# Optimization experiments

Hardware: AMD Instinct MI355X
Metric: run time of the kernel (lower is better)

## Reference

```python
import jax, jax.numpy as jnp
import numpy as np
from jax import lax


def _depthwise_conv1d(x, w, b):
    # x: [B, L, D]; w: [D, 1, KW]; b: [D]
    # Mirrors torch nn.Conv1d(D, D, kernel_size=4, groups=D, padding=3): output length L + 3.
    D = x.shape[-1]
    xt = jnp.transpose(x, (0, 2, 1))  # [B, D, L]
    out = lax.conv_general_dilated(
        xt, w, window_strides=(1,), padding=[(3, 3)],
        feature_group_count=D, dimension_numbers=('NCH', 'OIH', 'NCH'))
    return jnp.transpose(out + b[None, :, None], (0, 2, 1))  # [B, L+3, D]


def _forward(x, a_hat, W_U, W_B, b_B, W_C, b_C, W_d1, b_d1, W_d2, b_d2, D_skip, conv_w, conv_b):
    xc = _depthwise_conv1d(x, conv_w, conv_b)            # [B, Lc, D], Lc = L + 3
    Bsz, Lc, Dm = xc.shape
    S = a_hat.shape[0]
    # selective parameters (torch Linear: y = x @ W.T + b)
    dt_feat = jax.nn.silu(xc @ W_d1.T + b_d1)            # [B, Lc, R]
    delta = jax.nn.softplus(dt_feat @ W_d2.T + b_d2)     # [B, Lc, 1]
    logA = -jnp.exp(a_hat)                               # [S], log(A) <= 0
    A_t = jnp.exp(delta * logA)                          # [B, Lc, S] discretized transition
    u_t = xc @ W_U.T                                     # [B, Lc, S]
    B_t = (xc @ W_B.T + b_B) * u_t                       # [B, Lc, S]
    C_t = xc @ W_C.T + b_C                               # [B, Lc, S]

    # selective scan: h_t = A_t * h_{t-1} + B_t * u_t ; y_t = <C_t, h_t> + D_skip * u_t
    # state h is per-(batch, channel d): [B, D, S]
    def step(h, inp):
        A_l, B_l, C_l, u_l = inp                         # [B,S],[B,S],[B,S],[B,D]
        h = A_l[:, None, :] * h + B_l[:, None, :] * u_l[:, :, None]  # [B, D, S]
        y = jnp.einsum('bds,bs->bd', h, C_l) + D_skip[None, :] * u_l
        return h, y

    h0 = jnp.zeros((Bsz, Dm, S), dtype=xc.dtype)
    _, ys = lax.scan(step, h0, (jnp.swapaxes(A_t, 0, 1), jnp.swapaxes(B_t, 0, 1),
                                jnp.swapaxes(C_t, 0, 1), jnp.swapaxes(xc, 0, 1)))
    return jnp.swapaxes(ys, 0, 1)                        # [B, Lc, D]


def setup_inputs() -> dict:
    key = jax.random.key(0)
    ks = jax.random.split(key, 10)
    B, L, D, S, R, KW = 4, 2048, 1024, 64, 4, 4
    f = jnp.float32
    sc = 0.02
    return {
        'x': jax.random.normal(ks[0], (B, L, D), f),
        'a_hat': jax.random.normal(ks[1], (S,), f),
        'W_U': jax.random.normal(ks[2], (S, D), f) * sc,
        'W_B': jax.random.normal(ks[3], (S, D), f) * sc,
        'b_B': jnp.zeros((S,), f),
        'W_C': jax.random.normal(ks[4], (S, D), f) * sc,
        'b_C': jnp.zeros((S,), f),
        'W_d1': jax.random.normal(ks[5], (R, D), f) * sc,
        'b_d1': jnp.zeros((R,), f),
        'W_d2': jax.random.normal(ks[6], (1, R), f) * sc,
        'b_d2': jnp.zeros((1,), f),
        'D_skip': jax.random.normal(ks[7], (D,), f),
        'conv_w': jax.random.normal(ks[8], (D, 1, KW), f) * 0.25,
        'conv_b': jnp.zeros((D,), f),
    }


def reference(x, a_hat, W_U, W_B, b_B, W_C, b_C, W_d1, b_d1, W_d2, b_d2, D_skip, conv_w, conv_b):
    return _forward(x, a_hat, W_U, W_B, b_B, W_C, b_C, W_d1, b_d1, W_d2, b_d2, D_skip, conv_w, conv_b)
```

## Files before the change

kernel.cpp:

```cpp
#include <hip/hip_runtime.h>
#include <hip/hip_bf16.h>

namespace {
constexpr int kB   = 4;
constexpr int kL   = 2048;
constexpr int kLc  = 2051;
constexpr int kD   = 1024;
constexpr int kS   = 64;
constexpr int kM   = kB * kLc;
constexpr int kNR  = 256;
constexpr int kQ   = 32;
constexpr int kTC  = (kLc + kQ - 1) / kQ;
constexpr int kGA  = 514;
constexpr int kGT  = 16384;
}

typedef __attribute__((ext_vector_type(8))) short bf16x8;
typedef __attribute__((ext_vector_type(4))) float f32x4;
typedef __attribute__((ext_vector_type(8))) unsigned short u16x8;

__device__ __forceinline__ float siluf_(float v) {
  return v / (1.f + expf(-v));
}
__device__ __forceinline__ float softplusf_(float v) {
  return (v > 20.f) ? v : log1pf(expf(v));
}
__device__ __forceinline__ unsigned short f2bf_(float f) {
  unsigned u = __float_as_uint(f);
  unsigned r = u + 0x7FFF + ((u >> 16) & 1);
  return (unsigned short)(r >> 16);
}
__device__ __forceinline__ float bf2f_(unsigned short u) {
  return __uint_as_float(((unsigned)u) << 16);
}

__global__ __launch_bounds__(256) void conv_kernel(
    const float* __restrict__ x, const float* __restrict__ cw,
    const float* __restrict__ cb, unsigned short* __restrict__ xcp,
    unsigned short* __restrict__ xT,
    const float* __restrict__ W_U, const float* __restrict__ W_B,
    const float* __restrict__ W_C, const float* __restrict__ W_d1,
    unsigned short* __restrict__ wcp) {
  __shared__ unsigned short tileT[kQ][136];

  int tid = threadIdx.x;
  if (blockIdx.y == 8) {
    int bx = blockIdx.x;
    if (bx < 128) {
      int g = bx >> 3, kq = bx & 7;
      int c8 = tid & 15, r = tid >> 4;
      int n = g * 16 + r;
      int k = kq * 128 + c8 * 8;
      const float* src = nullptr;
      if (n < 64)        src = W_U + (size_t)n * kD;
      else if (n < 128)  src = W_B + (size_t)(n - 64) * kD;
      else if (n < 192)  src = W_C + (size_t)(n - 128) * kD;
      else if (n < 196)  src = W_d1 + (size_t)(n - 192) * kD;
      u16x8 o;
#pragma unroll
      for (int j = 0; j < 8; ++j)
        o[j] = src ? f2bf_(src[k + j]) : (unsigned short)0;
      size_t dst = (size_t)g * kGT + (size_t)(k >> 5) * 512 + r * 32 + (k & 31);
      *(u16x8*)(wcp + dst) = o;
    } else if (bx < 136) {
      u16x8 z = {0, 0, 0, 0, 0, 0, 0, 0};
      size_t off = (size_t)513 * kGT + (size_t)(bx - 128) * 2048 + (size_t)tid * 8;
      *(u16x8*)(xcp + off) = z;
    } else if (bx < 138) {
      int i = (bx - 136) * 256 + tid;
      int kt = i >> 4, rr = (i >> 2) & 3, k8 = i & 3;
      u16x8 z = {0, 0, 0, 0, 0, 0, 0, 0};
      size_t off = (size_t)512 * kGT + (size_t)kt * 512 + (12 + rr) * 32 + k8 * 8;
      *(u16x8*)(xcp + off) = z;
    }
    return;
  }

  int bc = blockIdx.x;
  int d0 = blockIdx.y * 128;
  int b = bc / kTC, c = bc % kTC;
  int t0 = c * kQ;
  int dl = tid & 127, tg = tid >> 7;
  int d = d0 + dl;

  float4 wv = *(const float4*)(cw + (size_t)d * 4);
  float bias = cb[d];
  int tstart = t0 + tg * 16;

  const float* xb = x + (size_t)b * kL * kD + d;
  auto ldx = [&](int t) -> float {
    return (t >= 0 && t < kL) ? xb[(size_t)t * kD] : 0.f;
  };
  float xm3 = ldx(tstart - 3);
  float xm2 = ldx(tstart - 2);
  float xm1 = ldx(tstart - 1);

  unsigned short vals[16];
#pragma unroll
  for (int j = 0; j < 16; ++j) {
    int t = tstart + j;
    float x0 = ldx(t);
    float o = bias + wv.x * xm3 + wv.y * xm2 + wv.z * xm1 + wv.w * x0;
    vals[j] = (t < kLc) ? f2bf_(o) : (unsigned short)0;
    tileT[tg * 16 + j][dl] = vals[j];
    xm3 = xm2; xm2 = xm1; xm1 = x0;
  }
#pragma unroll
  for (int j = 0; j < 16; ++j) {
    int t = tstart + j;
    if (t < kLc) {
      int bt = b * kLc + t;
      size_t po = (size_t)(bt >> 4) * kGT + (size_t)(d >> 5) * 512 +
                  (size_t)(bt & 15) * 32 + (d & 31);
      xcp[po] = vals[j];
    }
  }
  __syncthreads();
  {
    int d_l = tid >> 1, th = tid & 1;
    u16x8 o0, o1;
#pragma unroll
    for (int j = 0; j < 8; ++j) {
      o0[j] = tileT[th * 16 + j][d_l];
      o1[j] = tileT[th * 16 + 8 + j][d_l];
    }
    unsigned short* dst = xT + ((size_t)bc * kD + d0 + d_l) * kQ + th * 16;
    *(u16x8*)dst = o0;
    *(u16x8*)(dst + 8) = o1;
  }
}

__global__ __launch_bounds__(256) void gemm_mfma_kernel(
    const unsigned short* __restrict__ xcp,
    const unsigned short* __restrict__ wcp, float* __restrict__ raw) {
  int tid = threadIdx.x;
  int w = tid >> 6, lane = tid & 63;
  int m0 = blockIdx.x * 32 + (w >> 1) * 16;
  int n0 = (w & 1) * 128;
  int l15 = lane & 15, lk = lane >> 4;

  const unsigned short* ap =
      xcp + (size_t)(blockIdx.x * 2 + (w >> 1)) * kGT + l15 * 32 + lk * 8;
  const unsigned short* bp =
      wcp + (size_t)((w & 1) * 8) * kGT + l15 * 32 + lk * 8;

  f32x4 acc[8];
#pragma unroll
  for (int nf = 0; nf < 8; ++nf) acc[nf] = f32x4{0.f, 0.f, 0.f, 0.f};

  bf16x8 a = *(const bf16x8*)(ap);
  bf16x8 bfr[8];
#pragma unroll
  for (int nf = 0; nf < 8; ++nf)
    bfr[nf] = *(const bf16x8*)(bp + (size_t)nf * kGT);

  for (int kt = 1; kt < 32; ++kt) {
    bf16x8 an = *(const bf16x8*)(ap + kt * 512);
    bf16x8 bn[8];
#pragma unroll
    for (int nf = 0; nf < 8; ++nf)
      bn[nf] = *(const bf16x8*)(bp + (size_t)nf * kGT + kt * 512);
#pragma unroll
    for (int nf = 0; nf < 8; ++nf)
      acc[nf] = __builtin_amdgcn_mfma_f32_16x16x32_bf16(a, bfr[nf], acc[nf], 0, 0, 0);
    a = an;
#pragma unroll
    for (int nf = 0; nf < 8; ++nf) bfr[nf] = bn[nf];
  }
#pragma unroll
  for (int nf = 0; nf < 8; ++nf)
    acc[nf] = __builtin_amdgcn_mfma_f32_16x16x32_bf16(a, bfr[nf], acc[nf], 0, 0, 0);

  int crow0 = m0 + lk * 4;
#pragma unroll
  for (int nf = 0; nf < 8; ++nf) {
    int col = n0 + nf * 16 + l15;
#pragma unroll
    for (int r = 0; r < 4; ++r) {
      int row = crow0 + r;
      if (row < kM) raw[(size_t)row * kNR + col] = acc[nf][r];
    }
  }
}

__global__ __launch_bounds__(256) void passA_kernel(
    const float* __restrict__ raw,
    const float* __restrict__ b_B, const float* __restrict__ b_C,
    const float* __restrict__ b_d1, const float* __restrict__ W_d2,
    const float* __restrict__ b_d2, const float* __restrict__ a_hat,
    unsigned short* __restrict__ Gm, unsigned short* __restrict__ Ctb,
    unsigned short* __restrict__ Bpre, float* __restrict__ dec) {
  __shared__ __align__(16) float Cfl[32][68];
  __shared__ __align__(16) float BulT[64][36];
  __shared__ float deltal[32];
  __shared__ float Dloc[32];
  __shared__ float logAl[64];

  int tid = threadIdx.x;
  int bc = blockIdx.x;
  int b = bc / kTC, c = bc % kTC;
  int t0 = c * kQ;
  int clen = min(kQ, kLc - t0);

  if (tid < 64) logAl[tid] = -expf(a_hat[tid]);
  if (tid >= 64 && tid < 96) {
    int t = tid - 64;
    float r0 = 0.f, r1 = 0.f, r2 = 0.f, r3 = 0.f;
    if (t < clen) {
      const float* rp = raw + (size_t)(b * kLc + t0 + t) * kNR + 192;
      r0 = rp[0]; r1 = rp[1]; r2 = rp[2]; r3 = rp[3];
    }
    float f0 = siluf_(r0 + b_d1[0]);
    float f1 = siluf_(r1 + b_d1[1]);
    float f2 = siluf_(r2 + b_d1[2]);
    float f3 = siluf_(r3 + b_d1[3]);
    float z = fmaf(f0, W_d2[0],
              fmaf(f1, W_d2[1], fmaf(f2, W_d2[2], fmaf(f3, W_d2[3], b_d2[0]))));
    deltal[t] = softplusf_(z);
  }
  for (int p = 0; p < 8; ++p) {
    int idx = p * 256 + tid;
    int t = idx >> 6, s = idx & 63;
    float u = 0.f, rb = 0.f, rc = 0.f;
    if (t < clen) {
      const float* rp = raw + (size_t)(b * kLc + t0 + t) * kNR;
      u = rp[s]; rb = rp[64 + s]; rc = rp[128 + s];
    }
    BulT[s][t] = (rb + b_B[s]) * u;
    Cfl[t][s] = rc + b_C[s];
  }
  __syncthreads();
  if (tid < 32) {
    float sum = 0.f;
    for (int j = 0; j <= tid; ++j) sum += deltal[j];
    Dloc[tid] = sum;
  }
  __syncthreads();
  float Dend = Dloc[31];

  for (int p = 0; p < 8; ++p) {
    int idx = p * 256 + tid;
    int t = idx >> 6, s = idx & 63;
    Ctb[(size_t)bc * 2048 + t * kS + s] =
        f2bf_(Cfl[t][s] * __expf(Dloc[t] * logAl[s]));
  }
  for (int p = 0; p < 8; ++p) {
    int idx = p * 256 + tid;
    int s = idx >> 5, tau = idx & 31;
    Bpre[(size_t)bc * 2048 + s * kQ + tau] =
        f2bf_(BulT[s][tau] * __expf((Dend - Dloc[tau]) * logAl[s]));
  }
  if (tid < 64) dec[(size_t)bc * kS + tid] = __expf(Dend * logAl[tid]);
  for (int p = 0; p < 4; ++p) {
    int idx = p * 256 + tid;
    int t = idx >> 5, tau = idx & 31;
    float g = 0.f;
    if (tau <= t) {
      float dd = Dloc[t] - Dloc[tau];
      for (int s = 0; s < 64; ++s)
        g = fmaf(Cfl[t][s] * BulT[s][tau], __expf(dd * logAl[s]), g);
    }
    Gm[((size_t)bc * 32 + t) * kQ + tau] = f2bf_(g);
  }
}

__global__ __launch_bounds__(256) void scT_kernel(
    const unsigned short* __restrict__ Bpre, const unsigned short* __restrict__ xT,
    unsigned short* __restrict__ ScT) {
  __shared__ __align__(16) unsigned short Bprel[64][40];
  int tid = threadIdx.x;
  int bc = blockIdx.x;
  int dq = blockIdx.y;
  {
    int s = tid >> 2, c8 = (tid & 3) * 8;
    *(u16x8*)&Bprel[s][c8] = *(const u16x8*)(Bpre + (size_t)bc * 2048 + s * kQ + c8);
  }
  __syncthreads();
  int w = tid >> 6, lane = tid & 63;
  int l15 = lane & 15, lk = lane >> 4;
  bf16x8 bfr[4];
#pragma unroll
  for (int st = 0; st < 4; ++st)
    bfr[st] = *(const bf16x8*)&Bprel[st * 16 + l15][lk * 8];
  const unsigned short* xTb = xT + (size_t)bc * kD * kQ;
  unsigned short* so = ScT + (size_t)bc * kD * kS;
#pragma unroll
  for (int mt = 0; mt < 4; ++mt) {
    int d0t = dq * 256 + (w * 4 + mt) * 16;
    bf16x8 af = *(const bf16x8*)(xTb + (size_t)(d0t + l15) * kQ + lk * 8);
    f32x4 acc[4];
#pragma unroll
    for (int st = 0; st < 4; ++st) {
      f32x4 z = {0.f, 0.f, 0.f, 0.f};
      acc[st] = __builtin_amdgcn_mfma_f32_16x16x32_bf16(af, bfr[st], z, 0, 0, 0);
    }
#pragma unroll
    for (int st = 0; st < 4; ++st)
#pragma unroll
      for (int r = 0; r < 4; ++r)
        so[(size_t)(d0t + lk * 4 + r) * kS + st * 16 + l15] = f2bf_(acc[st][r]);
  }
}

__global__ __launch_bounds__(256) void chscan_kernel(
    const float* __restrict__ dec, unsigned short* __restrict__ Sc) {
  int bk = blockIdx.x >> 7;
  int part = blockIdx.x & 127;
  int p = part * 256 + threadIdx.x;
  int flat = p * 2;
  int s0 = flat & 63;
  const size_t cstride = (size_t)kS * kD;
  size_t base = (size_t)bk * kTC * cstride + flat;
  const float* decb = dec + (size_t)bk * kTC * kS + s0;
  float r0 = 0.f, r1 = 0.f;
  for (int c0 = 0; c0 < kTC; c0 += 16) {
    int n = kTC - c0;
    if (n > 16) n = 16;
    unsigned v[16];
    float2 dd[16];
#pragma unroll
    for (int j = 0; j < 16; ++j) {
      if (j < n) {
        v[j] = *(const unsigned*)(Sc + base + (size_t)(c0 + j) * cstride);
        dd[j] = *(const float2*)(decb + (size_t)(c0 + j) * kS);
      }
    }
#pragma unroll
    for (int j = 0; j < 16; ++j) {
      if (j < n) {
        unsigned ost = (unsigned)f2bf_(r0) | ((unsigned)f2bf_(r1) << 16);
        *(unsigned*)(Sc + base + (size_t)(c0 + j) * cstride) = ost;
        r0 = fmaf(dd[j].x, r0, bf2f_((unsigned short)(v[j] & 0xFFFF)));
        r1 = fmaf(dd[j].y, r1, bf2f_((unsigned short)(v[j] >> 16)));
      }
    }
  }
}

__global__ __launch_bounds__(256) void passB_kernel(
    const unsigned short* __restrict__ Gm, const unsigned short* __restrict__ Ctb,
    const unsigned short* __restrict__ xT, const unsigned short* __restrict__ hT,
    const float* __restrict__ D_skip, float* __restrict__ out) {
  int tid = threadIdx.x;
  int bc = blockIdx.x;
  int quarter = blockIdx.y;
  int b = bc / kTC, c = bc % kTC;
  int t0c = c * kQ;
  int clen = min(kQ, kLc - t0c);
  int w = tid >> 6, lane = tid & 63;
  int l15 = lane & 15, lk = lane >> 4;

  const unsigned short* Gb = Gm + (size_t)bc * 32 * kQ;
  bf16x8 aG0 = *(const bf16x8*)(Gb + (size_t)l15 * kQ + lk * 8);
  bf16x8 aG1 = *(const bf16x8*)(Gb + (size_t)(16 + l15) * kQ + lk * 8);
  const unsigned short* Cb = Ctb + (size_t)bc * 2048;
  bf16x8 aC0l = *(const bf16x8*)(Cb + (size_t)l15 * kS + lk * 8);
  bf16x8 aC0h = *(const bf16x8*)(Cb + (size_t)l15 * kS + 32 + lk * 8);
  bf16x8 aC1l = *(const bf16x8*)(Cb + (size_t)(16 + l15) * kS + lk * 8);
  bf16x8 aC1h = *(const bf16x8*)(Cb + (size_t)(16 + l15) * kS + 32 + lk * 8);

  const unsigned short* xTb = xT + (size_t)bc * kD * kQ;
  const unsigned short* hTb = hT + (size_t)bc * kD * kS;
  size_t rowbase = (size_t)b * kLc + t0c;
  int dbase = quarter * 256 + w * 64;

#pragma unroll
  for (int nt = 0; nt < 4; ++nt) {
    int d = dbase + nt * 16 + l15;
    bf16x8 bX  = *(const bf16x8*)(xTb + (size_t)d * kQ + lk * 8);
    bf16x8 bHl = *(const bf16x8*)(hTb + (size_t)d * kS + lk * 8);
    bf16x8 bHh = *(const bf16x8*)(hTb + (size_t)d * kS + 32 + lk * 8);
    f32x4 z = {0.f, 0.f, 0.f, 0.f};
    f32x4 accA = __builtin_amdgcn_mfma_f32_16x16x32_bf16(aC0l, bHl, z, 0, 0, 0);
    accA = __builtin_amdgcn_mfma_f32_16x16x32_bf16(aC0h, bHh, accA, 0, 0, 0);
    accA = __builtin_amdgcn_mfma_f32_16x16x32_bf16(aG0, bX, accA, 0, 0, 0);
    f32x4 accB = __builtin_amdgcn_mfma_f32_16x16x32_bf16(aC1l, bHl, z, 0, 0, 0);
    accB = __builtin_amdgcn_mfma_f32_16x16x32_bf16(aC1h, bHh, accB, 0, 0, 0);
    accB = __builtin_amdgcn_mfma_f32_16x16x32_bf16(aG1, bX, accB, 0, 0, 0);

    float ds = D_skip[d];
    ushort4 xa = *(const ushort4*)(xTb + (size_t)d * kQ + lk * 4);
    ushort4 xb = *(const ushort4*)(xTb + (size_t)d * kQ + 16 + lk * 4);
    const unsigned short* xap = (const unsigned short*)&xa;
    const unsigned short* xbp = (const unsigned short*)&xb;
#pragma unroll
    for (int r = 0; r < 4; ++r) {
      int t = lk * 4 + r;
      if (t < clen)
        out[(rowbase + t) * kD + d] = fmaf(ds, bf2f_(xap[r]), accA[r]);
      int t2 = 16 + lk * 4 + r;
      if (t2 < clen)
        out[(rowbase + t2) * kD + d] = fmaf(ds, bf2f_(xbp[r]), accB[r]);
    }
  }
}

extern "C" void kernel_launch(void* const* d_in, const int* in_sizes, int n_in,
                              void* d_out, int out_size, void* d_ws, size_t ws_size,
                              hipStream_t stream) {
  const float* x      = (const float*)d_in[0];
  const float* a_hat  = (const float*)d_in[1];
  const float* W_U    = (const float*)d_in[2];
  const float* W_B    = (const float*)d_in[3];
  const float* b_B    = (const float*)d_in[4];
  const float* W_C    = (const float*)d_in[5];
  const float* b_C    = (const float*)d_in[6];
  const float* W_d1   = (const float*)d_in[7];
  const float* b_d1   = (const float*)d_in[8];
  const float* W_d2   = (const float*)d_in[9];
  const float* b_d2   = (const float*)d_in[10];
  const float* D_skip = (const float*)d_in[11];
  const float* conv_w = (const float*)d_in[12];
  const float* conv_b = (const float*)d_in[13];
  float* out = (float*)d_out;

  char* w = (char*)d_ws;
  auto nextp = [&](size_t bytes) {
    char* p = w;
    w += (bytes + 255) & ~(size_t)255;
    return p;
  };
  unsigned short* xcp  = (unsigned short*)nextp((size_t)kGA * kGT * 2);
  unsigned short* wcp  = (unsigned short*)nextp((size_t)16 * kGT * 2);
  unsigned short* xT   = (unsigned short*)nextp((size_t)kB * kTC * kD * kQ * 2);
  float*          raw  = (float*)nextp((size_t)kM * kNR * 4);
  unsigned short* Gm   = (unsigned short*)nextp((size_t)kB * kTC * 32 * kQ * 2);
  unsigned short* Ctb  = (unsigned short*)nextp((size_t)kB * kTC * 2048 * 2);
  unsigned short* Bpre = (unsigned short*)nextp((size_t)kB * kTC * 2048 * 2);
  float*          dec  = (float*)nextp((size_t)kB * kTC * kS * 4);
  unsigned short* ScT  = (unsigned short*)nextp((size_t)kB * kTC * kD * kS * 2);

  dim3 cgrid(kB * kTC, 9);
  conv_kernel<<<cgrid, 256, 0, stream>>>(x, conv_w, conv_b, xcp, xT,
                                         W_U, W_B, W_C, W_d1, wcp);

  gemm_mfma_kernel<<<(kM + 31) / 32, 256, 0, stream>>>(xcp, wcp, raw);

  passA_kernel<<<kB * kTC, 256, 0, stream>>>(
      raw, b_B, b_C, b_d1, W_d2, b_d2, a_hat, Gm, Ctb, Bpre, dec);

  dim3 sgrid(kB * kTC, 4);
  scT_kernel<<<sgrid, 256, 0, stream>>>(Bpre, xT, ScT);

  chscan_kernel<<<kB * 128, 256, 0, stream>>>(dec, ScT);

  dim3 bgrid(kB * kTC, 4);
  passB_kernel<<<bgrid, 256, 0, stream>>>(Gm, Ctb, xT, ScT, D_skip, out);
}
```

Baseline: 111.1 us.

## Double scan chunk length from 32 to 64 timesteps across all kernels

Raises the chunk size of the chunked selective scan from 32 to 64 and rewrites the conv, passA, scT and passB kernels to match: longer per-thread conv runs, larger shared tiles, two-step MFMA K accumulation over 64 timesteps, and four M-tiles per block in passB. This halves the number of chunks, which shrinks the inter-chunk state scan and the ScT state traffic (bf16 [D,S] per chunk). In exchange the intra-chunk G matrix costs four times as much per chunk (twice as much overall), and register pressure in passB rises. The conv grid is pinned at 138 blocks with an early-exit guard, because the weight-packing branch needs those block indices while there are now fewer chunks.

```diff
diff --git a/kernel.cpp b/kernel.cpp
--- a/kernel.cpp
+++ b/kernel.cpp
@@ -9,7 +9,7 @@
 constexpr int kS   = 64;
 constexpr int kM   = kB * kLc;
 constexpr int kNR  = 256;
-constexpr int kQ   = 32;
+constexpr int kQ   = 64;
 constexpr int kTC  = (kLc + kQ - 1) / kQ;
 constexpr int kGA  = 514;
 constexpr int kGT  = 16384;
@@ -77,6 +77,7 @@
   }
 
   int bc = blockIdx.x;
+  if (bc >= kB * kTC) return;
   int d0 = blockIdx.y * 128;
   int b = bc / kTC, c = bc % kTC;
   int t0 = c * kQ;
@@ -85,7 +86,7 @@
 
   float4 wv = *(const float4*)(cw + (size_t)d * 4);
   float bias = cb[d];
-  int tstart = t0 + tg * 16;
+  int tstart = t0 + tg * 32;
 
   const float* xb = x + (size_t)b * kL * kD + d;
   auto ldx = [&](int t) -> float {
@@ -95,18 +96,18 @@
   float xm2 = ldx(tstart - 2);
   float xm1 = ldx(tstart - 1);
 
-  unsigned short vals[16];
-#pragma unroll
-  for (int j = 0; j < 16; ++j) {
+  unsigned short vals[32];
+#pragma unroll
+  for (int j = 0; j < 32; ++j) {
     int t = tstart + j;
     float x0 = ldx(t);
     float o = bias + wv.x * xm3 + wv.y * xm2 + wv.z * xm1 + wv.w * x0;
     vals[j] = (t < kLc) ? f2bf_(o) : (unsigned short)0;
-    tileT[tg * 16 + j][dl] = vals[j];
+    tileT[tg * 32 + j][dl] = vals[j];
     xm3 = xm2; xm2 = xm1; xm1 = x0;
   }
 #pragma unroll
-  for (int j = 0; j < 16; ++j) {
+  for (int j = 0; j < 32; ++j) {
     int t = tstart + j;
     if (t < kLc) {
       int bt = b * kLc + t;
@@ -118,15 +119,14 @@
   __syncthreads();
   {
     int d_l = tid >> 1, th = tid & 1;
-    u16x8 o0, o1;
-#pragma unroll
-    for (int j = 0; j < 8; ++j) {
-      o0[j] = tileT[th * 16 + j][d_l];
-      o1[j] = tileT[th * 16 + 8 + j][d_l];
-    }
-    unsigned short* dst = xT + ((size_t)bc * kD + d0 + d_l) * kQ + th * 16;
-    *(u16x8*)dst = o0;
-    *(u16x8*)(dst + 8) = o1;
+    unsigned short* dst = xT + ((size_t)bc * kD + d0 + d_l) * kQ + th * 32;
+#pragma unroll
+    for (int q = 0; q < 4; ++q) {
+      u16x8 o;
+#pragma unroll
+      for (int j = 0; j < 8; ++j) o[j] = tileT[th * 32 + q * 8 + j][d_l];
+      *(u16x8*)(dst + q * 8) = o;
+    }
   }
 }
 
@@ -190,11 +190,11 @@
     const float* __restrict__ b_d2, const float* __restrict__ a_hat,
     unsigned short* __restrict__ Gm, unsigned short* __restrict__ Ctb,
     unsigned short* __restrict__ Bpre, float* __restrict__ dec) {
-  __shared__ __align__(16) float Cfl[32][68];
-  __shared__ __align__(16) float BulT[64][36];
-  __shared__ float deltal[32];
-  __shared__ float Dloc[32];
-  __shared__ float logAl[64];
+  __shared__ __align__(16) float Cfl[kQ][68];
+  __shared__ __align__(16) float BulT[kS][72];
+  __shared__ float deltal[kQ];
+  __shared__ float Dloc[kQ];
+  __shared__ float logAl[kS];
 
   int tid = threadIdx.x;
   int bc = blockIdx.x;
@@ -203,7 +203,7 @@
   int clen = min(kQ, kLc - t0);
 
   if (tid < 64) logAl[tid] = -expf(a_hat[tid]);
-  if (tid >= 64 && tid < 96) {
+  if (tid >= 64 && tid < 128) {
     int t = tid - 64;
     float r0 = 0.f, r1 = 0.f, r2 = 0.f, r3 = 0.f;
     if (t < clen) {
@@ -218,7 +218,7 @@
               fmaf(f1, W_d2[1], fmaf(f2, W_d2[2], fmaf(f3, W_d2[3], b_d2[0]))));
     deltal[t] = softplusf_(z);
   }
-  for (int p = 0; p < 8; ++p) {
+  for (int p = 0; p < 16; ++p) {
     int idx = p * 256 + tid;
     int t = idx >> 6, s = idx & 63;
     float u = 0.f, rb = 0.f, rc = 0.f;
@@ -230,75 +230,78 @@
     Cfl[t][s] = rc + b_C[s];
   }
   __syncthreads();
-  if (tid < 32) {
+  if (tid < 64) {
     float sum = 0.f;
     for (int j = 0; j <= tid; ++j) sum += deltal[j];
     Dloc[tid] = sum;
   }
   __syncthreads();
-  float Dend = Dloc[31];
-
-  for (int p = 0; p < 8; ++p) {
+  float Dend = Dloc[kQ - 1];
+
+  for (int p = 0; p < 16; ++p) {
     int idx = p * 256 + tid;
     int t = idx >> 6, s = idx & 63;
-    Ctb[(size_t)bc * 2048 + t * kS + s] =
+    Ctb[(size_t)bc * 4096 + t * kS + s] =
         f2bf_(Cfl[t][s] * __expf(Dloc[t] * logAl[s]));
   }
-  for (int p = 0; p < 8; ++p) {
+  for (int p = 0; p < 16; ++p) {
     int idx = p * 256 + tid;
-    int s = idx >> 5, tau = idx & 31;
-    Bpre[(size_t)bc * 2048 + s * kQ + tau] =
+    int s = idx >> 6, tau = idx & 63;
+    Bpre[(size_t)bc * 4096 + s * kQ + tau] =
         f2bf_(BulT[s][tau] * __expf((Dend - Dloc[tau]) * logAl[s]));
   }
   if (tid < 64) dec[(size_t)bc * kS + tid] = __expf(Dend * logAl[tid]);
-  for (int p = 0; p < 4; ++p) {
+  for (int p = 0; p < 16; ++p) {
     int idx = p * 256 + tid;
-    int t = idx >> 5, tau = idx & 31;
+    int t = idx >> 6, tau = idx & 63;
     float g = 0.f;
     if (tau <= t) {
       float dd = Dloc[t] - Dloc[tau];
       for (int s = 0; s < 64; ++s)
         g = fmaf(Cfl[t][s] * BulT[s][tau], __expf(dd * logAl[s]), g);
     }
-    Gm[((size_t)bc * 32 + t) * kQ + tau] = f2bf_(g);
+    Gm[(size_t)bc * 4096 + t * kQ + tau] = f2bf_(g);
   }
 }
 
 __global__ __launch_bounds__(256) void scT_kernel(
     const unsigned short* __restrict__ Bpre, const unsigned short* __restrict__ xT,
     unsigned short* __restrict__ ScT) {
-  __shared__ __align__(16) unsigned short Bprel[64][40];
+  __shared__ __align__(16) unsigned short Bprel[64][72];
   int tid = threadIdx.x;
   int bc = blockIdx.x;
   int dq = blockIdx.y;
-  {
-    int s = tid >> 2, c8 = (tid & 3) * 8;
-    *(u16x8*)&Bprel[s][c8] = *(const u16x8*)(Bpre + (size_t)bc * 2048 + s * kQ + c8);
+#pragma unroll
+  for (int rr = 0; rr < 2; ++rr) {
+    int i = rr * 256 + tid;
+    int s = i >> 3, c8 = (i & 7) * 8;
+    *(u16x8*)&Bprel[s][c8] = *(const u16x8*)(Bpre + (size_t)bc * 4096 + s * kQ + c8);
   }
   __syncthreads();
   int w = tid >> 6, lane = tid & 63;
   int l15 = lane & 15, lk = lane >> 4;
-  bf16x8 bfr[4];
+  bf16x8 bfr[4][2];
 #pragma unroll
   for (int st = 0; st < 4; ++st)
-    bfr[st] = *(const bf16x8*)&Bprel[st * 16 + l15][lk * 8];
+#pragma unroll
+    for (int h = 0; h < 2; ++h)
+      bfr[st][h] = *(const bf16x8*)&Bprel[st * 16 + l15][h * 32 + lk * 8];
   const unsigned short* xTb = xT + (size_t)bc * kD * kQ;
   unsigned short* so = ScT + (size_t)bc * kD * kS;
 #pragma unroll
   for (int mt = 0; mt < 4; ++mt) {
     int d0t = dq * 256 + (w * 4 + mt) * 16;
-    bf16x8 af = *(const bf16x8*)(xTb + (size_t)(d0t + l15) * kQ + lk * 8);
-    f32x4 acc[4];
+    bf16x8 af0 = *(const bf16x8*)(xTb + (size_t)(d0t + l15) * kQ + lk * 8);
+    bf16x8 af1 = *(const bf16x8*)(xTb + (size_t)(d0t + l15) * kQ + 32 + lk * 8);
 #pragma unroll
     for (int st = 0; st < 4; ++st) {
       f32x4 z = {0.f, 0.f, 0.f, 0.f};
-      acc[st] = __builtin_amdgcn_mfma_f32_16x16x32_bf16(af, bfr[st], z, 0, 0, 0);
-    }
-#pragma unroll
-    for (int st = 0; st < 4; ++st)
+      f32x4 acc = __builtin_amdgcn_mfma_f32_16x16x32_bf16(af0, bfr[st][0], z, 0, 0, 0);
+      acc = __builtin_amdgcn_mfma_f32_16x16x32_bf16(af1, bfr[st][1], acc, 0, 0, 0);
 #pragma unroll
       for (int r = 0; r < 4; ++r)
-        so[(size_t)(d0t + lk * 4 + r) * kS + st * 16 + l15] = f2bf_(acc[st][r]);
+        so[(size_t)(d0t + lk * 4 + r) * kS + st * 16 + l15] = f2bf_(acc[r]);
+    }
   }
 }
 
@@ -350,14 +353,16 @@
   int w = tid >> 6, lane = tid & 63;
   int l15 = lane & 15, lk = lane >> 4;
 
-  const unsigned short* Gb = Gm + (size_t)bc * 32 * kQ;
-  bf16x8 aG0 = *(const bf16x8*)(Gb + (size_t)l15 * kQ + lk * 8);
-  bf16x8 aG1 = *(const bf16x8*)(Gb + (size_t)(16 + l15) * kQ + lk * 8);
-  const unsigned short* Cb = Ctb + (size_t)bc * 2048;
-  bf16x8 aC0l = *(const bf16x8*)(Cb + (size_t)l15 * kS + lk * 8);
-  bf16x8 aC0h = *(const bf16x8*)(Cb + (size_t)l15 * kS + 32 + lk * 8);
-  bf16x8 aC1l = *(const bf16x8*)(Cb + (size_t)(16 + l15) * kS + lk * 8);
-  bf16x8 aC1h = *(const bf16x8*)(Cb + (size_t)(16 + l15) * kS + 32 + lk * 8);
+  const unsigned short* Gb = Gm + (size_t)bc * 4096;
+  const unsigned short* Cb = Ctb + (size_t)bc * 4096;
+  bf16x8 aG[4][2], aC[4][2];
+#pragma unroll
+  for (int mt = 0; mt < 4; ++mt)
+#pragma unroll
+    for (int h = 0; h < 2; ++h) {
+      aG[mt][h] = *(const bf16x8*)(Gb + (size_t)(mt * 16 + l15) * kQ + h * 32 + lk * 8);
+      aC[mt][h] = *(const bf16x8*)(Cb + (size_t)(mt * 16 + l15) * kS + h * 32 + lk * 8);
+    }
 
   const unsigned short* xTb = xT + (size_t)bc * kD * kQ;
   const unsigned short* hTb = hT + (size_t)bc * kD * kS;
@@ -367,30 +372,27 @@
 #pragma unroll
   for (int nt = 0; nt < 4; ++nt) {
     int d = dbase + nt * 16 + l15;
-    bf16x8 bX  = *(const bf16x8*)(xTb + (size_t)d * kQ + lk * 8);
-    bf16x8 bHl = *(const bf16x8*)(hTb + (size_t)d * kS + lk * 8);
-    bf16x8 bHh = *(const bf16x8*)(hTb + (size_t)d * kS + 32 + lk * 8);
-    f32x4 z = {0.f, 0.f, 0.f, 0.f};
-    f32x4 accA = __builtin_amdgcn_mfma_f32_16x16x32_bf16(aC0l, bHl, z, 0, 0, 0);
-    accA = __builtin_amdgcn_mfma_f32_16x16x32_bf16(aC0h, bHh, accA, 0, 0, 0);
-    accA = __builtin_amdgcn_mfma_f32_16x16x32_bf16(aG0, bX, accA, 0, 0, 0);
-    f32x4 accB = __builtin_amdgcn_mfma_f32_16x16x32_bf16(aC1l, bHl, z, 0, 0, 0);
-    accB = __builtin_amdgcn_mfma_f32_16x16x32_bf16(aC1h, bHh, accB, 0, 0, 0);
-    accB = __builtin_amdgcn_mfma_f32_16x16x32_bf16(aG1, bX, accB, 0, 0, 0);
-
+    bf16x8 bX0 = *(const bf16x8*)(xTb + (size_t)d * kQ + lk * 8);
+    bf16x8 bX1 = *(const bf16x8*)(xTb + (size_t)d * kQ + 32 + lk * 8);
+    bf16x8 bH0 = *(const bf16x8*)(hTb + (size_t)d * kS + lk * 8);
+    bf16x8 bH1 = *(const bf16x8*)(hTb + (size_t)d * kS + 32 + lk * 8);
     float ds = D_skip[d];
-    ushort4 xa = *(const ushort4*)(xTb + (size_t)d * kQ + lk * 4);
-    ushort4 xb = *(const ushort4*)(xTb + (size_t)d * kQ + 16 + lk * 4);
-    const unsigned short* xap = (const unsigned short*)&xa;
-    const unsigned short* xbp = (const unsigned short*)&xb;
-#pragma unroll
-    for (int r = 0; r < 4; ++r) {
-      int t = lk * 4 + r;
-      if (t < clen)
-        out[(rowbase + t) * kD + d] = fmaf(ds, bf2f_(xap[r]), accA[r]);
-      int t2 = 16 + lk * 4 + r;
-      if (t2 < clen)
-        out[(rowbase + t2) * kD + d] = fmaf(ds, bf2f_(xbp[r]), accB[r]);
+#pragma unroll
+    for (int mt = 0; mt < 4; ++mt) {
+      f32x4 z = {0.f, 0.f, 0.f, 0.f};
+      f32x4 acc = __builtin_amdgcn_mfma_f32_16x16x32_bf16(aC[mt][0], bH0, z, 0, 0, 0);
+      acc = __builtin_amdgcn_mfma_f32_16x16x32_bf16(aC[mt][1], bH1, acc, 0, 0, 0);
+      acc = __builtin_amdgcn_mfma_f32_16x16x32_bf16(aG[mt][0], bX0, acc, 0, 0, 0);
+      acc = __builtin_amdgcn_mfma_f32_16x16x32_bf16(aG[mt][1], bX1, acc, 0, 0, 0);
+
+      ushort4 xa = *(const ushort4*)(xTb + (size_t)d * kQ + mt * 16 + lk * 4);
+      const unsigned short* xap = (const unsigned short*)&xa;
+#pragma unroll
+      for (int r = 0; r < 4; ++r) {
+        int t = mt * 16 + lk * 4 + r;
+        if (t < clen)
+          out[(rowbase + t) * kD + d] = fmaf(ds, bf2f_(xap[r]), acc[r]);
+      }
     }
   }
 }
@@ -424,13 +426,13 @@
   unsigned short* wcp  = (unsigned short*)nextp((size_t)16 * kGT * 2);
   unsigned short* xT   = (unsigned short*)nextp((size_t)kB * kTC * kD * kQ * 2);
   float*          raw  = (float*)nextp((size_t)kM * kNR * 4);
-  unsigned short* Gm   = (unsigned short*)nextp((size_t)kB * kTC * 32 * kQ * 2);
-  unsigned short* Ctb  = (unsigned short*)nextp((size_t)kB * kTC * 2048 * 2);
-  unsigned short* Bpre = (unsigned short*)nextp((size_t)kB * kTC * 2048 * 2);
+  unsigned short* Gm   = (unsigned short*)nextp((size_t)kB * kTC * 4096 * 2);
+  unsigned short* Ctb  = (unsigned short*)nextp((size_t)kB * kTC * 4096 * 2);
+  unsigned short* Bpre = (unsigned short*)nextp((size_t)kB * kTC * 4096 * 2);
   float*          dec  = (float*)nextp((size_t)kB * kTC * kS * 4);
   unsigned short* ScT  = (unsigned short*)nextp((size_t)kB * kTC * kD * kS * 2);
 
-  dim3 cgrid(kB * kTC, 9);
+  dim3 cgrid(138, 9);
   conv_kernel<<<cgrid, 256, 0, stream>>>(x, conv_w, conv_b, xcp, xT,
                                          W_U, W_B, W_C, W_d1, wcp);
 
```

Result: slower. 138.7 us (+24.8%).
